# Kernel tuning notes

Hardware: AMD Instinct MI355X
Metric: run time of the kernel (lower is better)

## Reference

```python
import jax, jax.numpy as jnp
from jax import lax
import numpy as np

N, D, K, T, E, S = 2048, 128, 16, 16, 8192, 256
GAMMA, SIGMA, TEMP, EPS = 0.1, 1.0, 1.0, 1e-10


def _xavier(k, out_d, in_d):
    lim = (6.0 / (in_d + out_d)) ** 0.5
    return jax.random.uniform(k, (out_d, in_d), minval=-lim, maxval=lim, dtype=jnp.float32)


def setup_inputs() -> dict:
    key = jax.random.key(0)
    ks = jax.random.split(key, 24)
    inp = {
        'edges': jax.random.randint(ks[0], (T, E, 2), 0, N, dtype=jnp.int32),
        'subject_idx': 3,
        'eps_phi': jax.random.normal(ks[1], (T, N, D), dtype=jnp.float32),
        'eps_beta': jax.random.normal(ks[2], (T, K, D), dtype=jnp.float32),
        'u_gumbel': jax.random.uniform(ks[3], (T, 2 * E, K), dtype=jnp.float32),
        'alpha_mean_emb': jax.random.normal(ks[4], (S, D), dtype=jnp.float32),
        'alpha_std_emb': jax.random.normal(ks[5], (S, D), dtype=jnp.float32),
        'W_s2phi': _xavier(ks[6], N * D, D), 'b_s2phi': jnp.zeros((N * D,), jnp.float32),
        'W_s2beta': _xavier(ks[7], K * D, D), 'b_s2beta': jnp.zeros((K * D,), jnp.float32),
        'W_bmean': _xavier(ks[8], D, D), 'b_bmean': jnp.zeros((D,), jnp.float32),
        'W_bstd': _xavier(ks[9], D, D), 'b_bstd': jnp.zeros((D,), jnp.float32),
        'W_pmean': _xavier(ks[10], D, D), 'b_pmean': jnp.zeros((D,), jnp.float32),
        'W_pstd': _xavier(ks[11], D, D), 'b_pstd': jnp.zeros((D,), jnp.float32),
        'W_pi': _xavier(ks[12], K, D),
        'Wih_n': 0.1 * jax.random.normal(ks[13], (3 * D, 2 * D), dtype=jnp.float32),
        'Whh_n': 0.1 * jax.random.normal(ks[14], (3 * D, D), dtype=jnp.float32),
        'bih_n': jnp.zeros((3 * D,), jnp.float32), 'bhh_n': jnp.zeros((3 * D,), jnp.float32),
        'Wih_c': 0.1 * jax.random.normal(ks[15], (3 * D, 2 * D), dtype=jnp.float32),
        'Whh_c': 0.1 * jax.random.normal(ks[16], (3 * D, D), dtype=jnp.float32),
        'bih_c': jnp.zeros((3 * D,), jnp.float32), 'bhh_c': jnp.zeros((3 * D,), jnp.float32),
        'W_dec': _xavier(ks[17], N, D),
    }
    return inp


def _gru(x, h, Wih, Whh, bih, bhh):
    # torch nn.GRU single-step cell (gate order r, z, n)
    gi = x @ Wih.T + bih
    gh = h @ Whh.T + bhh
    i_r, i_z, i_n = jnp.split(gi, 3, axis=-1)
    h_r, h_z, h_n = jnp.split(gh, 3, axis=-1)
    r = jax.nn.sigmoid(i_r + h_r)
    z = jax.nn.sigmoid(i_z + h_z)
    n = jnp.tanh(i_n + r * h_n)
    return (1.0 - z) * n + z * h


def _kld_gauss(m1, s1, m2, s2):
    # KL(N(m1,s1) || N(m2,s2)), s2 scalar
    return 0.5 * jnp.sum(2.0 * (jnp.log(s2) - jnp.log(s1)) + (s1 ** 2 + (m1 - m2) ** 2) / (s2 ** 2) - 1.0)


def reference(edges, subject_idx, eps_phi, eps_beta, u_gumbel,
              alpha_mean_emb, alpha_std_emb, W_s2phi, b_s2phi, W_s2beta, b_s2beta,
              W_bmean, b_bmean, W_bstd, b_bstd, W_pmean, b_pmean, W_pstd, b_pstd,
              W_pi, Wih_n, Whh_n, bih_n, bhh_n, Wih_c, Whh_c, bih_c, bhh_c, W_dec):
    a_m = alpha_mean_emb[subject_idx]
    a_s = jax.nn.softplus(alpha_std_emb[subject_idx])
    kld_alpha = _kld_gauss(a_m, a_s, jnp.zeros_like(a_m), 1.0)
    phi0 = (a_m @ W_s2phi.T + b_s2phi).reshape(N, D)
    beta0 = (a_m @ W_s2beta.T + b_s2beta).reshape(K, D)

    def step(carry, xs):
        h_phi, h_beta, phi_prior, beta_prior = carry
        e_t, ep, eb, u = xs
        w = jnp.concatenate([e_t[:, 0], e_t[:, 1]])  # [2E]
        c = jnp.concatenate([e_t[:, 1], e_t[:, 0]])  # [2E]
        h_phi = _gru(jnp.concatenate([phi_prior, phi_prior], -1), h_phi, Wih_n, Whh_n, bih_n, bhh_n)
        h_beta = _gru(jnp.concatenate([beta_prior, beta_prior], -1), h_beta, Wih_c, Whh_c, bih_c, bhh_c)
        beta_mean = h_beta @ W_bmean.T + b_bmean
        beta_std = jax.nn.softplus(h_beta @ W_bstd.T + b_bstd)
        phi_mean = h_phi @ W_pmean.T + b_pmean
        phi_std = jax.nn.softplus(h_phi @ W_pstd.T + b_pstd)
        beta_s = beta_mean + beta_std * eb  # [K, D]
        phi_s = phi_mean + phi_std * ep     # [N, D]
        logits_q = (phi_s[w] * phi_s[c]) @ W_pi.T        # [2E, K] posterior logits
        log_post = jax.nn.log_softmax(logits_q, axis=-1)
        post = jnp.exp(log_post)
        log_prior = jax.nn.log_softmax(phi_s[w] @ beta_s.T, axis=-1)  # p(z|w)
        g = -jnp.log(-jnp.log(u + EPS) + EPS)  # gumbel noise
        z = jax.nn.softmax((logits_q + g) / TEMP, axis=-1)  # soft gumbel-softmax sample
        recon_logp = jax.nn.log_softmax((z @ beta_s) @ W_dec.T, axis=-1)  # [2E, N]
        nll = -jnp.sum(jnp.take_along_axis(recon_logp, c[:, None], axis=1))
        kld_z = jnp.sum(post * (log_post - log_prior))
        kld_beta = _kld_gauss(beta_mean, beta_std, beta_prior, GAMMA)
        kld_phi = _kld_gauss(phi_mean, phi_std, phi_prior, SIGMA)
        return (h_phi, h_beta, phi_s, beta_s), jnp.stack([nll, kld_z, kld_beta, kld_phi])

    carry0 = (jnp.zeros((N, D), jnp.float32), jnp.zeros((K, D), jnp.float32), phi0, beta0)
    _, per_t = lax.scan(step, carry0, (edges, eps_phi, eps_beta, u_gumbel))
    sums = per_t.sum(axis=0)  # [nll, kld_z, kld_beta, kld_phi]
    cnt = jnp.float32(T * 2 * E)
    out = jnp.stack([sums[0], sums[1], T * kld_alpha, sums[2], sums[3]]) / cnt
    return out  # [nll, kld_z, kld_alpha, kld_beta, kld_phi]
```

## Files before the change

kernel.cpp:

```cpp
#include <hip/hip_runtime.h>

#define NN 2048
#define DD 128
#define KK 16
#define TT 16
#define EE 8192
#define TWOE 16384
#define CNT 262144.0f

#define LOG2E 1.4426950408889634f
#define LN2   0.6931471805599453f

__device__ __forceinline__ float exp2_(float x) { return __builtin_amdgcn_exp2f(x); }
__device__ __forceinline__ float log2_(float x) { return __builtin_amdgcn_logf(x); }
__device__ __forceinline__ float expf_(float x) { return exp2_(x * LOG2E); }
__device__ __forceinline__ float logf_(float x) { return log2_(x) * LN2; }
__device__ __forceinline__ float sigmoidf_(float x) { return 1.f / (1.f + expf_(-x)); }
__device__ __forceinline__ float softplusf_(float x) { return fmaxf(x, 0.f) + logf_(1.f + expf_(-fabsf(x))); }
__device__ __forceinline__ float tanhf_(float x) { return 1.f - 2.f / (1.f + expf_(2.f * x)); }

#define D4(a,b) ((a).x*(b).x + (a).y*(b).y + (a).z*(b).z + (a).w*(b).w)

__launch_bounds__(256)
__global__ void prep_kernel(const float* __restrict__ Wih_n, const float* __restrict__ Whh_n,
                            const float* __restrict__ Wih_c, const float* __restrict__ Whh_c,
                            const float* __restrict__ W_pmean, const float* __restrict__ W_pstd,
                            const float* __restrict__ W_bmean, const float* __restrict__ W_bstd,
                            float* __restrict__ Bg_n, float* __restrict__ Bg_c,
                            float* __restrict__ Bms_n, float* __restrict__ Bms_c)
{
    int idx = blockIdx.x * 256 + threadIdx.x;
    if (idx < 98304) {
        int r = idx;
        if (r < 49152) { int j = r >> 7, k2 = r & 127; Bg_n[r] = Wih_n[j*256 + k2] + Wih_n[j*256 + 128 + k2]; }
        else Bg_n[r] = Whh_n[r - 49152];
    } else if (idx < 196608) {
        int r = idx - 98304;
        if (r < 49152) { int j = r >> 7, k2 = r & 127; Bg_c[r] = Wih_c[j*256 + k2] + Wih_c[j*256 + 128 + k2]; }
        else Bg_c[r] = Whh_c[r - 49152];
    } else if (idx < 229376) {
        int r = idx - 196608;
        Bms_n[r] = (r < 16384) ? W_pmean[r] : W_pstd[r - 16384];
    } else {
        int r = idx - 229376;
        Bms_c[r] = (r < 16384) ? W_bmean[r] : W_bstd[r - 16384];
    }
}

__launch_bounds__(128)
__global__ void alpha_kernel(const float* __restrict__ amE, const float* __restrict__ asE,
                             const int* __restrict__ sidx, float* __restrict__ a_m, float* __restrict__ acc)
{
    __shared__ float red[128];
    int d = threadIdx.x;
    int s = sidx[0];
    float am = amE[s*128 + d];
    float as = softplusf_(asE[s*128 + d]);
    a_m[d] = am;
    float e = -logf_(as) + 0.5f*(as*as + am*am) - 0.5f;
    red[d] = e; __syncthreads();
    for (int st = 64; st > 0; st >>= 1) { if (d < st) red[d] += red[d + st]; __syncthreads(); }
    if (d == 0) acc[2] = red[0];
}

__launch_bounds__(256)
__global__ void phi0_kernel(const float* __restrict__ Wp, const float* __restrict__ bp,
                            const float* __restrict__ Wb, const float* __restrict__ bb,
                            const float* __restrict__ a_m, float* __restrict__ phi0, float* __restrict__ beta0)
{
    int wid = threadIdx.x >> 6, l = threadIdx.x & 63;
    long long row = (long long)blockIdx.x * 4 + wid;
    const float* W; const float* b; float* o; long long r = row;
    if (row < 262144) { W = Wp; b = bp; o = phi0; }
    else { W = Wb; b = bb; o = beta0; r = row - 262144; }
    const float* wr = W + r * 128;
    float acc = a_m[l] * wr[l] + a_m[64 + l] * wr[64 + l];
    #pragma unroll
    for (int m = 32; m >= 1; m >>= 1) acc += __shfl_xor(acc, m);
    if (l == 0) o[r] = acc + b[r];
}

__launch_bounds__(256)
__global__ void gemm_bias(const float* __restrict__ Ap1, const float* __restrict__ Ap2,
                          const float* __restrict__ Ab1, const float* __restrict__ Ab2,
                          const float* __restrict__ Bphi, const float* __restrict__ Bbeta,
                          const float* __restrict__ b0p, const float* __restrict__ b1p,
                          const float* __restrict__ b0b, const float* __restrict__ b1b,
                          float* __restrict__ Cphi, float* __restrict__ Cbeta,
                          int Ncols, int Nsplit, int MtPhi, int Mbeta)
{
    __shared__ float As[32][68];
    __shared__ float Bs[32][68];
    bool isBeta = (blockIdx.y == (unsigned)MtPhi);
    int n0 = blockIdx.x * 64;
    const float* A = isBeta ? ((n0 >= Nsplit) ? Ab2 : Ab1) : ((n0 >= Nsplit) ? Ap2 : Ap1);
    const float* B = isBeta ? Bbeta : Bphi;
    const float* b0 = isBeta ? b0b : b0p;
    const float* b1 = isBeta ? b1b : b1p;
    float* C = isBeta ? Cbeta : Cphi;
    int M = isBeta ? Mbeta : MtPhi * 64;
    int m0 = isBeta ? 0 : blockIdx.y * 64;
    int tid = threadIdx.x;
    int tx = tid & 15, ty = tid >> 4;
    float accu[4][4] = {};
    int lr = tid >> 2;
    int lk = (tid & 3) * 8;
    for (int k0 = 0; k0 < 128; k0 += 32) {
        int arow = m0 + lr;
        const float* ap = A + (size_t)arow * 128 + k0 + lk;
        const float* bp = B + (size_t)(n0 + lr) * 128 + k0 + lk;
        #pragma unroll
        for (int qq = 0; qq < 8; ++qq) {
            As[lk + qq][lr] = (arow < M) ? ap[qq] : 0.f;
            Bs[lk + qq][lr] = bp[qq];
        }
        __syncthreads();
        #pragma unroll
        for (int kk = 0; kk < 32; ++kk) {
            float av[4], bv[4];
            #pragma unroll
            for (int i2 = 0; i2 < 4; ++i2) av[i2] = As[kk][ty*4 + i2];
            #pragma unroll
            for (int j2 = 0; j2 < 4; ++j2) bv[j2] = Bs[kk][tx*4 + j2];
            #pragma unroll
            for (int i2 = 0; i2 < 4; ++i2)
                #pragma unroll
                for (int j2 = 0; j2 < 4; ++j2)
                    accu[i2][j2] = fmaf(av[i2], bv[j2], accu[i2][j2]);
        }
        __syncthreads();
    }
    #pragma unroll
    for (int i2 = 0; i2 < 4; ++i2) {
        int row = m0 + ty*4 + i2;
        if (row >= M) continue;
        #pragma unroll
        for (int j2 = 0; j2 < 4; ++j2) {
            int col = n0 + tx*4 + j2;
            float bv = (col < Nsplit) ? b0[col] : b1[col - Nsplit];
            C[(size_t)row * Ncols + col] = accu[i2][j2] + bv;
        }
    }
}

__launch_bounds__(256)
__global__ void gates_kernel(const float* __restrict__ Gphi, const float* __restrict__ Gbeta,
                             float* __restrict__ h_phi, float* __restrict__ h_beta)
{
    long long idx = (long long)blockIdx.x * 256 + threadIdx.x;
    const float* G; float* h; int i, jj;
    if (idx < 262144) { i = (int)(idx >> 7); jj = (int)(idx & 127); G = Gphi; h = h_phi; }
    else { int r = (int)(idx - 262144); i = r >> 7; jj = r & 127; G = Gbeta; h = h_beta; }
    const float* g = G + (size_t)i * 768;
    float r_ = sigmoidf_(g[jj] + g[384 + jj]);
    float z_ = sigmoidf_(g[128 + jj] + g[512 + jj]);
    float n_ = tanhf_(g[256 + jj] + r_ * g[640 + jj]);
    int hi = i * 128 + jj;
    h[hi] = (1.f - z_) * n_ + z_ * h[hi];
}

__launch_bounds__(256)
__global__ void sample_kernel(const float* __restrict__ MSphi, const float* __restrict__ MSbeta,
                              const float* __restrict__ epsP, const float* __restrict__ epsB,
                              const float* __restrict__ phiPrior, const float* __restrict__ betaPrior,
                              float* __restrict__ phiS, float* __restrict__ betaS, float* __restrict__ acc)
{
    __shared__ float red[256];
    int tid = threadIdx.x;
    long long idx = (long long)blockIdx.x * 256 + tid;
    float elem; int target;
    if (idx < 262144) {
        int i = (int)(idx >> 7), jj = (int)(idx & 127);
        float mean = MSphi[(size_t)i*256 + jj];
        float stdv = softplusf_(MSphi[(size_t)i*256 + 128 + jj]);
        float sv = mean + stdv * epsP[idx];
        phiS[idx] = sv;
        float d = mean - phiPrior[idx];
        elem = -logf_(stdv) + 0.5f*(stdv*stdv + d*d) - 0.5f;
        target = 4;
    } else {
        int r = (int)(idx - 262144);
        int i = r >> 7, jj = r & 127;
        float mean = MSbeta[i*256 + jj];
        float stdv = softplusf_(MSbeta[i*256 + 128 + jj]);
        float sv = mean + stdv * epsB[r];
        betaS[r] = sv;
        float d = mean - betaPrior[r];
        elem = (-2.3025850929940457f - logf_(stdv)) + 50.0f*(stdv*stdv + d*d) - 0.5f;
        target = 3;
    }
    red[tid] = elem; __syncthreads();
    for (int st = 128; st > 0; st >>= 1) { if (tid < st) red[tid] += red[tid + st]; __syncthreads(); }
    if (tid == 0) atomicAdd(acc + target, red[0]);
}

__launch_bounds__(256)
__global__ void mt_kernel(const float* __restrict__ betaS, const float* __restrict__ W_dec, float* __restrict__ Mt)
{
    int tid = threadIdx.x, wid = tid >> 6, l = tid & 63;
    int n = blockIdx.x * 4 + wid;
    int k = l & 15, q = l >> 4;
    const float* bs = betaS + k*128 + q*32;
    const float* wd = W_dec + (size_t)n*128 + q*32;
    float p = 0.f;
    #pragma unroll
    for (int j = 0; j < 32; ++j) p = fmaf(bs[j], wd[j], p);
    p += __shfl_xor(p, 16);
    p += __shfl_xor(p, 32);
    if (l < 16) Mt[n*16 + l] = p * LOG2E;
}

#define ZSTEP(A,B,Wv,Bv) { float4 a_=(A), b_=(B); \
    lp += a_.x*(Bv).x + a_.y*(Bv).y + a_.z*(Bv).z + a_.w*(Bv).w; \
    lq += (a_.x*b_.x)*(Wv).x + (a_.y*b_.y)*(Wv).y + (a_.z*b_.z)*(Wv).z + (a_.w*b_.w)*(Wv).w; }

__launch_bounds__(256, 3)
__global__ void z_kernel(const float* __restrict__ phiS, const float* __restrict__ betaS,
                         const float* __restrict__ W_pi, const int* __restrict__ edges_t,
                         const float* __restrict__ u_t, float* __restrict__ Z, float* __restrict__ acc)
{
    int tid = threadIdx.x, wid = tid >> 6, l = tid & 63;
    int k = l >> 2, q = l & 3;
    int d0 = q * 32;
    const float4* wp = (const float4*)(W_pi  + k*128 + d0);
    const float4* bp = (const float4*)(betaS + k*128 + d0);
    float4 wr0 = wp[0], wr1 = wp[1], wr2 = wp[2], wr3 = wp[3],
           wr4 = wp[4], wr5 = wp[5], wr6 = wp[6], wr7 = wp[7];
    float4 br0 = bp[0], br1 = bp[1], br2 = bp[2], br3 = bp[3],
           br4 = bp[4], br5 = bp[5], br6 = bp[6], br7 = bp[7];
    float kz = 0.f;
    int gw = blockIdx.x * 4 + wid;
    for (int it = 0; it < 8; ++it) {
        int j = gw * 8 + it;
        int e = j & 8191; int fl = j >> 13;
        int w = edges_t[e*2 + fl], c = edges_t[e*2 + (fl ^ 1)];
        const float4* pw4 = (const float4*)(phiS + w*128 + d0);
        const float4* pc4 = (const float4*)(phiS + c*128 + d0);
        float lq = 0.f, lp = 0.f;
        ZSTEP(pw4[0], pc4[0], wr0, br0); ZSTEP(pw4[1], pc4[1], wr1, br1);
        ZSTEP(pw4[2], pc4[2], wr2, br2); ZSTEP(pw4[3], pc4[3], wr3, br3);
        ZSTEP(pw4[4], pc4[4], wr4, br4); ZSTEP(pw4[5], pc4[5], wr5, br5);
        ZSTEP(pw4[6], pc4[6], wr6, br6); ZSTEP(pw4[7], pc4[7], wr7, br7);
        lq += __shfl_xor(lq, 1); lq += __shfl_xor(lq, 2);
        lp += __shfl_xor(lp, 1); lp += __shfl_xor(lp, 2);
        float eq = expf_(lq);
        float sq = eq;
        sq += __shfl_xor(sq, 4); sq += __shfl_xor(sq, 8); sq += __shfl_xor(sq, 16); sq += __shfl_xor(sq, 32);
        float rsq = __builtin_amdgcn_rcpf(sq);
        float logpost = lq - logf_(sq);
        float post = eq * rsq;
        float mp = lp;
        mp = fmaxf(mp, __shfl_xor(mp, 4));  mp = fmaxf(mp, __shfl_xor(mp, 8));
        mp = fmaxf(mp, __shfl_xor(mp, 16)); mp = fmaxf(mp, __shfl_xor(mp, 32));
        float ep = expf_(lp - mp);
        float sp = ep;
        sp += __shfl_xor(sp, 4); sp += __shfl_xor(sp, 8); sp += __shfl_xor(sp, 16); sp += __shfl_xor(sp, 32);
        float logprior = (lp - mp) - logf_(sp);
        float v = post * (logpost - logprior);
        v += __shfl_xor(v, 4); v += __shfl_xor(v, 8); v += __shfl_xor(v, 16); v += __shfl_xor(v, 32);
        kz += v;
        float u = u_t[(size_t)j*16 + k];
        float g = -logf_(-logf_(u + 1e-10f) + 1e-10f);
        float zl = lq + g;
        float ez = expf_(zl);
        float sz = ez;
        sz += __shfl_xor(sz, 4); sz += __shfl_xor(sz, 8); sz += __shfl_xor(sz, 16); sz += __shfl_xor(sz, 32);
        if (q == 0) Z[(size_t)j*16 + k] = ez * __builtin_amdgcn_rcpf(sz);
    }
    if (l == 0) atomicAdd(acc + 1, kz);
}

__launch_bounds__(512, 3)
__global__ void nll_kernel(const float* __restrict__ Mt, const float* __restrict__ Z,
                           const int* __restrict__ edges_t, float* __restrict__ acc)
{
    __shared__ float ss[32][8], sc[32][8];
    int tid = threadIdx.x, wid = tid >> 6, l = tid & 63;
    int n0 = tid * 4;
    const float4* mp = (const float4*)(Mt + (size_t)n0 * 16);
    float4 M0 = mp[0],  M1 = mp[1],  M2 = mp[2],  M3 = mp[3];
    float4 M4 = mp[4],  M5 = mp[5],  M6 = mp[6],  M7 = mp[7];
    float4 M8 = mp[8],  M9 = mp[9],  M10 = mp[10], M11 = mp[11];
    float4 M12 = mp[12], M13 = mp[13], M14 = mp[14], M15 = mp[15];
    for (int e = 0; e < 32; ++e) {
        int j = blockIdx.x * 32 + e;
        int ei = j & 8191; int fl = j >> 13;
        int c = edges_t[ei*2 + (fl ^ 1)];
        const float4* zp = (const float4*)(Z + (size_t)j * 16);
        float4 Z0 = zp[0], Z1 = zp[1], Z2 = zp[2], Z3 = zp[3];
        float v0 = D4(Z0, M0)  + D4(Z1, M1)  + D4(Z2, M2)  + D4(Z3, M3);
        float v1 = D4(Z0, M4)  + D4(Z1, M5)  + D4(Z2, M6)  + D4(Z3, M7);
        float v2 = D4(Z0, M8)  + D4(Z1, M9)  + D4(Z2, M10) + D4(Z3, M11);
        float v3 = D4(Z0, M12) + D4(Z1, M13) + D4(Z2, M14) + D4(Z3, M15);
        float s = exp2_(v0) + exp2_(v1) + exp2_(v2) + exp2_(v3);
        float cv = 0.f;
        cv = (c == n0    ) ? v0 : cv;
        cv = (c == n0 + 1) ? v1 : cv;
        cv = (c == n0 + 2) ? v2 : cv;
        cv = (c == n0 + 3) ? v3 : cv;
        #pragma unroll
        for (int m = 1; m < 64; m <<= 1) {
            s  += __shfl_xor(s, m);
            cv += __shfl_xor(cv, m);
        }
        if (l == 0) { ss[e][wid] = s; sc[e][wid] = cv; }
    }
    __syncthreads();
    float val = 0.f;
    if (tid < 32) {
        float S = 0.f, CV = 0.f;
        #pragma unroll
        for (int w2 = 0; w2 < 8; ++w2) { S += ss[tid][w2]; CV += sc[tid][w2]; }
        val = LN2 * (log2_(S) - CV);
    }
    if (tid < 64) {
        #pragma unroll
        for (int m = 1; m < 64; m <<= 1) val += __shfl_xor(val, m);
        if (tid == 0) atomicAdd(acc + 0, val);
    }
}

__global__ void final_kernel(const float* __restrict__ acc, float* __restrict__ out)
{
    if (threadIdx.x == 0 && blockIdx.x == 0) {
        out[0] = acc[0] / CNT;
        out[1] = acc[1] / CNT;
        out[2] = 16.f * acc[2] / CNT;
        out[3] = acc[3] / CNT;
        out[4] = acc[4] / CNT;
    }
}

extern "C" void kernel_launch(void* const* d_in, const int* in_sizes, int n_in,
                              void* d_out, int out_size, void* d_ws, size_t ws_size,
                              hipStream_t stream)
{
    (void)in_sizes; (void)n_in; (void)out_size; (void)ws_size;
    const int*   edges   = (const int*)d_in[0];
    const int*   sidx    = (const int*)d_in[1];
    const float* eps_phi = (const float*)d_in[2];
    const float* eps_beta= (const float*)d_in[3];
    const float* u_g     = (const float*)d_in[4];
    const float* amE     = (const float*)d_in[5];
    const float* asE     = (const float*)d_in[6];
    const float* W_s2phi = (const float*)d_in[7];
    const float* b_s2phi = (const float*)d_in[8];
    const float* W_s2beta= (const float*)d_in[9];
    const float* b_s2beta= (const float*)d_in[10];
    const float* W_bmean = (const float*)d_in[11];
    const float* b_bmean = (const float*)d_in[12];
    const float* W_bstd  = (const float*)d_in[13];
    const float* b_bstd  = (const float*)d_in[14];
    const float* W_pmean = (const float*)d_in[15];
    const float* b_pmean = (const float*)d_in[16];
    const float* W_pstd  = (const float*)d_in[17];
    const float* b_pstd  = (const float*)d_in[18];
    const float* W_pi    = (const float*)d_in[19];
    const float* Wih_n   = (const float*)d_in[20];
    const float* Whh_n   = (const float*)d_in[21];
    const float* bih_n   = (const float*)d_in[22];
    const float* bhh_n   = (const float*)d_in[23];
    const float* Wih_c   = (const float*)d_in[24];
    const float* Whh_c   = (const float*)d_in[25];
    const float* bih_c   = (const float*)d_in[26];
    const float* bhh_c   = (const float*)d_in[27];
    const float* W_dec   = (const float*)d_in[28];

    float* ws     = (float*)d_ws;
    float* Bg_n   = ws;
    float* Bg_c   = Bg_n   + 98304;
    float* Bms_n  = Bg_c   + 98304;
    float* Bms_c  = Bms_n  + 32768;
    float* a_m    = Bms_c  + 32768;
    float* phiA   = a_m    + 128;
    float* phiB   = phiA   + 262144;
    float* h_phi  = phiB   + 262144;
    float* betaA  = h_phi  + 262144;
    float* betaB  = betaA  + 2048;
    float* h_beta = betaB  + 2048;
    float* Gphi   = h_beta + 2048;
    float* Gbeta  = Gphi   + 1572864;
    float* MSphi  = Gbeta  + 12288;
    float* MSbeta = MSphi  + 524288;
    float* Mt     = MSbeta + 4096;
    float* Zb     = Mt     + 32768;
    float* acc    = Zb     + 262144;

    (void)hipMemsetAsync(h_phi,  0, 262144 * sizeof(float), stream);
    (void)hipMemsetAsync(h_beta, 0, 2048 * sizeof(float), stream);
    (void)hipMemsetAsync(acc,    0, 8 * sizeof(float), stream);

    prep_kernel<<<1024, 256, 0, stream>>>(Wih_n, Whh_n, Wih_c, Whh_c,
                                          W_pmean, W_pstd, W_bmean, W_bstd,
                                          Bg_n, Bg_c, Bms_n, Bms_c);
    alpha_kernel<<<1, 128, 0, stream>>>(amE, asE, sidx, a_m, acc);
    phi0_kernel<<<66048, 256, 0, stream>>>(W_s2phi, b_s2phi, W_s2beta, b_s2beta, a_m, phiA, betaA);

    float* phiPrior = phiA;  float* phiS = phiB;
    float* betaPrior = betaA; float* betaS = betaB;
    for (int t = 0; t < TT; ++t) {
        gemm_bias<<<dim3(12, 33), 256, 0, stream>>>(phiPrior, h_phi, betaPrior, h_beta,
                                                    Bg_n, Bg_c, bih_n, bhh_n, bih_c, bhh_c,
                                                    Gphi, Gbeta, 768, 384, 32, 16);
        gates_kernel<<<1032, 256, 0, stream>>>(Gphi, Gbeta, h_phi, h_beta);
        gemm_bias<<<dim3(4, 33), 256, 0, stream>>>(h_phi, h_phi, h_beta, h_beta,
                                                   Bms_n, Bms_c, b_pmean, b_pstd, b_bmean, b_bstd,
                                                   MSphi, MSbeta, 256, 128, 32, 16);
        sample_kernel<<<1032, 256, 0, stream>>>(MSphi, MSbeta,
                                                eps_phi + (size_t)t * 262144, eps_beta + (size_t)t * 2048,
                                                phiPrior, betaPrior, phiS, betaS, acc);
        mt_kernel<<<512, 256, 0, stream>>>(betaS, W_dec, Mt);
        z_kernel<<<512, 256, 0, stream>>>(phiS, betaS, W_pi,
                                          edges + (size_t)t * EE * 2, u_g + (size_t)t * TWOE * KK, Zb, acc);
        nll_kernel<<<512, 512, 0, stream>>>(Mt, Zb, edges + (size_t)t * EE * 2, acc);
        float* tp = phiPrior; phiPrior = phiS; phiS = tp;
        float* tb = betaPrior; betaPrior = betaS; betaS = tb;
    }
    final_kernel<<<1, 64, 0, stream>>>(acc, (float*)d_out);
}
```

Measured before the change: 2.682 ms.

## Fuse GRU gemm with gates, mean/std gemm with sampling, and z with nll

The per-step pipeline drops from seven kernels to four. The GRU input and hidden GEMMs are now fused with the gate nonlinearity, with ping-pong hidden buffers. The mean/std GEMM is fused with reparameterised sampling and the KL reduction. The z and nll kernels are merged so soft samples stay in shared memory, and the alpha, prep and memset setup work is folded into one init kernel. This removes the large G, MS and Z global intermediates and several launches per step. The trade-off is that the fused GEMMs launch only 132 blocks each, which lowers parallelism.

```diff
diff --git a/kernel.cpp b/kernel.cpp
--- a/kernel.cpp
+++ b/kernel.cpp
@@ -22,14 +22,36 @@
 #define D4(a,b) ((a).x*(b).x + (a).y*(b).y + (a).z*(b).z + (a).w*(b).w)
 
 __launch_bounds__(256)
-__global__ void prep_kernel(const float* __restrict__ Wih_n, const float* __restrict__ Whh_n,
+__global__ void init_kernel(const float* __restrict__ Wih_n, const float* __restrict__ Whh_n,
                             const float* __restrict__ Wih_c, const float* __restrict__ Whh_c,
                             const float* __restrict__ W_pmean, const float* __restrict__ W_pstd,
                             const float* __restrict__ W_bmean, const float* __restrict__ W_bstd,
                             float* __restrict__ Bg_n, float* __restrict__ Bg_c,
-                            float* __restrict__ Bms_n, float* __restrict__ Bms_c)
-{
+                            float* __restrict__ Bms_n, float* __restrict__ Bms_c,
+                            float* __restrict__ hphiA, float* __restrict__ hbetaA,
+                            const float* __restrict__ amE, const float* __restrict__ asE,
+                            const int* __restrict__ sidx, float* __restrict__ a_m,
+                            float* __restrict__ acc)
+{
+    if (blockIdx.x == 1024) {
+        __shared__ float red[128];
+        int d = threadIdx.x;
+        if (d < 128) {
+            int s = sidx[0];
+            float am = amE[s*128 + d];
+            float as = softplusf_(asE[s*128 + d]);
+            a_m[d] = am;
+            red[d] = -logf_(as) + 0.5f*(as*as + am*am) - 0.5f;
+        }
+        __syncthreads();
+        for (int st = 64; st > 0; st >>= 1) { if (d < st) red[d] += red[d + st]; __syncthreads(); }
+        if (d == 0) acc[2] = red[0];
+        return;
+    }
     int idx = blockIdx.x * 256 + threadIdx.x;
+    hphiA[idx] = 0.f;
+    if (idx < 2048) hbetaA[idx] = 0.f;
+    if (idx < 2) { acc[idx] = 0.f; acc[idx + 3] = 0.f; }
     if (idx < 98304) {
         int r = idx;
         if (r < 49152) { int j = r >> 7, k2 = r & 127; Bg_n[r] = Wih_n[j*256 + k2] + Wih_n[j*256 + 128 + k2]; }
@@ -47,22 +69,6 @@
     }
 }
 
-__launch_bounds__(128)
-__global__ void alpha_kernel(const float* __restrict__ amE, const float* __restrict__ asE,
-                             const int* __restrict__ sidx, float* __restrict__ a_m, float* __restrict__ acc)
-{
-    __shared__ float red[128];
-    int d = threadIdx.x;
-    int s = sidx[0];
-    float am = amE[s*128 + d];
-    float as = softplusf_(asE[s*128 + d]);
-    a_m[d] = am;
-    float e = -logf_(as) + 0.5f*(as*as + am*am) - 0.5f;
-    red[d] = e; __syncthreads();
-    for (int st = 64; st > 0; st >>= 1) { if (d < st) red[d] += red[d + st]; __syncthreads(); }
-    if (d == 0) acc[2] = red[0];
-}
-
 __launch_bounds__(256)
 __global__ void phi0_kernel(const float* __restrict__ Wp, const float* __restrict__ bp,
                             const float* __restrict__ Wb, const float* __restrict__ bb,
@@ -81,117 +87,172 @@
 }
 
 __launch_bounds__(256)
-__global__ void gemm_bias(const float* __restrict__ Ap1, const float* __restrict__ Ap2,
-                          const float* __restrict__ Ab1, const float* __restrict__ Ab2,
-                          const float* __restrict__ Bphi, const float* __restrict__ Bbeta,
-                          const float* __restrict__ b0p, const float* __restrict__ b1p,
-                          const float* __restrict__ b0b, const float* __restrict__ b1b,
-                          float* __restrict__ Cphi, float* __restrict__ Cbeta,
-                          int Ncols, int Nsplit, int MtPhi, int Mbeta)
-{
-    __shared__ float As[32][68];
-    __shared__ float Bs[32][68];
-    bool isBeta = (blockIdx.y == (unsigned)MtPhi);
-    int n0 = blockIdx.x * 64;
-    const float* A = isBeta ? ((n0 >= Nsplit) ? Ab2 : Ab1) : ((n0 >= Nsplit) ? Ap2 : Ap1);
-    const float* B = isBeta ? Bbeta : Bphi;
-    const float* b0 = isBeta ? b0b : b0p;
-    const float* b1 = isBeta ? b1b : b1p;
-    float* C = isBeta ? Cbeta : Cphi;
-    int M = isBeta ? Mbeta : MtPhi * 64;
-    int m0 = isBeta ? 0 : blockIdx.y * 64;
+__global__ void gru_kernel(const float* __restrict__ phiPrior, const float* __restrict__ betaPrior,
+                           const float* __restrict__ hPhiOld, float* __restrict__ hPhiNew,
+                           const float* __restrict__ hBetaOld, float* __restrict__ hBetaNew,
+                           const float* __restrict__ Bg_n, const float* __restrict__ Bg_c,
+                           const float* __restrict__ bih_n, const float* __restrict__ bhh_n,
+                           const float* __restrict__ bih_c, const float* __restrict__ bhh_c)
+{
+    __shared__ float Xs[32][64];
+    __shared__ float Hs[32][64];
+    __shared__ float Ws[32][192];
+    int bx = blockIdx.x;
+    const float* X; const float* Hold; float* Hnew; const float* Bg; const float* bih; const float* bhh;
+    int m0, M, j0;
+    if (bx < 128) {
+        m0 = (bx >> 2) * 64; j0 = (bx & 3) * 32; M = 2048;
+        X = phiPrior; Hold = hPhiOld; Hnew = hPhiNew; Bg = Bg_n; bih = bih_n; bhh = bhh_n;
+    } else {
+        m0 = 0; j0 = (bx - 128) * 32; M = 16;
+        X = betaPrior; Hold = hBetaOld; Hnew = hBetaNew; Bg = Bg_c; bih = bih_c; bhh = bhh_c;
+    }
     int tid = threadIdx.x;
-    int tx = tid & 15, ty = tid >> 4;
-    float accu[4][4] = {};
-    int lr = tid >> 2;
-    int lk = (tid & 3) * 8;
+    int j  = tid & 31;
+    int rr = tid >> 5;
+    float acc[6][8] = {};
+    int srow = tid >> 3;
+    int skq  = (tid & 7) * 4;
     for (int k0 = 0; k0 < 128; k0 += 32) {
-        int arow = m0 + lr;
-        const float* ap = A + (size_t)arow * 128 + k0 + lk;
-        const float* bp = B + (size_t)(n0 + lr) * 128 + k0 + lk;
-        #pragma unroll
-        for (int qq = 0; qq < 8; ++qq) {
-            As[lk + qq][lr] = (arow < M) ? ap[qq] : 0.f;
-            Bs[lk + qq][lr] = bp[qq];
+        #pragma unroll
+        for (int h2 = 0; h2 < 2; ++h2) {
+            int row = srow + 32 * h2;
+            int grow = m0 + row;
+            float4 xv = make_float4(0.f,0.f,0.f,0.f), hv = xv;
+            if (grow < M) {
+                xv = *(const float4*)(X    + (size_t)grow*128 + k0 + skq);
+                hv = *(const float4*)(Hold + (size_t)grow*128 + k0 + skq);
+            }
+            Xs[skq+0][row] = xv.x; Xs[skq+1][row] = xv.y; Xs[skq+2][row] = xv.z; Xs[skq+3][row] = xv.w;
+            Hs[skq+0][row] = hv.x; Hs[skq+1][row] = hv.y; Hs[skq+2][row] = hv.z; Hs[skq+3][row] = hv.w;
+        }
+        #pragma unroll
+        for (int h6 = 0; h6 < 6; ++h6) {
+            int rowIdx = srow + 32 * h6;
+            int g = rowIdx >> 5, jj2 = rowIdx & 31;
+            float4 wv = *(const float4*)(Bg + (size_t)(g*128 + j0 + jj2)*128 + k0 + skq);
+            Ws[skq+0][rowIdx] = wv.x; Ws[skq+1][rowIdx] = wv.y; Ws[skq+2][rowIdx] = wv.z; Ws[skq+3][rowIdx] = wv.w;
         }
         __syncthreads();
         #pragma unroll
         for (int kk = 0; kk < 32; ++kk) {
-            float av[4], bv[4];
+            float xa[8], ha[8];
+            *(float4*)&xa[0] = *(const float4*)&Xs[kk][rr*8];
+            *(float4*)&xa[4] = *(const float4*)&Xs[kk][rr*8+4];
+            *(float4*)&ha[0] = *(const float4*)&Hs[kk][rr*8];
+            *(float4*)&ha[4] = *(const float4*)&Hs[kk][rr*8+4];
             #pragma unroll
-            for (int i2 = 0; i2 < 4; ++i2) av[i2] = As[kk][ty*4 + i2];
+            for (int g = 0; g < 3; ++g) {
+                float wv = Ws[kk][g*32 + j];
+                #pragma unroll
+                for (int i = 0; i < 8; ++i) acc[g][i] = fmaf(xa[i], wv, acc[g][i]);
+            }
             #pragma unroll
-            for (int j2 = 0; j2 < 4; ++j2) bv[j2] = Bs[kk][tx*4 + j2];
+            for (int g = 3; g < 6; ++g) {
+                float wv = Ws[kk][g*32 + j];
+                #pragma unroll
+                for (int i = 0; i < 8; ++i) acc[g][i] = fmaf(ha[i], wv, acc[g][i]);
+            }
+        }
+        __syncthreads();
+    }
+    float bi_r = bih[j0 + j], bi_z = bih[128 + j0 + j], bi_n = bih[256 + j0 + j];
+    float bh_r = bhh[j0 + j], bh_z = bhh[128 + j0 + j], bh_n = bhh[256 + j0 + j];
+    #pragma unroll
+    for (int i = 0; i < 8; ++i) {
+        int row = m0 + rr*8 + i;
+        if (row < M) {
+            float r_ = sigmoidf_(acc[0][i] + bi_r + acc[3][i] + bh_r);
+            float z_ = sigmoidf_(acc[1][i] + bi_z + acc[4][i] + bh_z);
+            float n_ = tanhf_(acc[2][i] + bi_n + r_ * (acc[5][i] + bh_n));
+            size_t hi = (size_t)row * 128 + j0 + j;
+            Hnew[hi] = (1.f - z_) * n_ + z_ * Hold[hi];
+        }
+    }
+}
+
+__launch_bounds__(256)
+__global__ void ms_kernel(const float* __restrict__ hPhi, const float* __restrict__ hBeta,
+                          const float* __restrict__ Bms_n, const float* __restrict__ Bms_c,
+                          const float* __restrict__ b_pmean, const float* __restrict__ b_pstd,
+                          const float* __restrict__ b_bmean, const float* __restrict__ b_bstd,
+                          const float* __restrict__ epsP, const float* __restrict__ epsB,
+                          const float* __restrict__ phiPrior, const float* __restrict__ betaPrior,
+                          float* __restrict__ phiS, float* __restrict__ betaS, float* __restrict__ acc)
+{
+    __shared__ float Hs[32][64];
+    __shared__ float Wms[32][64];
+    __shared__ float red[256];
+    int bx = blockIdx.x;
+    const float* H; const float* Bms; const float* bm; const float* bs;
+    const float* eps; const float* prior; float* out;
+    int m0, M, j0; bool isPhi;
+    if (bx < 128) {
+        m0 = (bx >> 2) * 64; j0 = (bx & 3) * 32; M = 2048; isPhi = true;
+        H = hPhi; Bms = Bms_n; bm = b_pmean; bs = b_pstd; eps = epsP; prior = phiPrior; out = phiS;
+    } else {
+        m0 = 0; j0 = (bx - 128) * 32; M = 16; isPhi = false;
+        H = hBeta; Bms = Bms_c; bm = b_bmean; bs = b_bstd; eps = epsB; prior = betaPrior; out = betaS;
+    }
+    int tid = threadIdx.x;
+    int j  = tid & 31;
+    int rr = tid >> 5;
+    float accM[8] = {}, accS[8] = {};
+    int srow = tid >> 3;
+    int skq  = (tid & 7) * 4;
+    for (int k0 = 0; k0 < 128; k0 += 32) {
+        #pragma unroll
+        for (int h2 = 0; h2 < 2; ++h2) {
+            int row = srow + 32 * h2;
+            int grow = m0 + row;
+            float4 hv = make_float4(0.f,0.f,0.f,0.f);
+            if (grow < M) hv = *(const float4*)(H + (size_t)grow*128 + k0 + skq);
+            Hs[skq+0][row] = hv.x; Hs[skq+1][row] = hv.y; Hs[skq+2][row] = hv.z; Hs[skq+3][row] = hv.w;
+        }
+        {
+            int rowIdx = srow + 32 * 0;
             #pragma unroll
-            for (int i2 = 0; i2 < 4; ++i2)
-                #pragma unroll
-                for (int j2 = 0; j2 < 4; ++j2)
-                    accu[i2][j2] = fmaf(av[i2], bv[j2], accu[i2][j2]);
+            for (int h2 = 0; h2 < 2; ++h2) {
+                int ri = rowIdx + 32 * h2;
+                int grp = ri >> 5, jj2 = ri & 31;
+                float4 wv = *(const float4*)(Bms + (size_t)(grp*128 + j0 + jj2)*128 + k0 + skq);
+                Wms[skq+0][ri] = wv.x; Wms[skq+1][ri] = wv.y; Wms[skq+2][ri] = wv.z; Wms[skq+3][ri] = wv.w;
+            }
         }
         __syncthreads();
-    }
+        #pragma unroll
+        for (int kk = 0; kk < 32; ++kk) {
+            float hv[8];
+            *(float4*)&hv[0] = *(const float4*)&Hs[kk][rr*8];
+            *(float4*)&hv[4] = *(const float4*)&Hs[kk][rr*8+4];
+            float wm = Wms[kk][j];
+            float ws = Wms[kk][32 + j];
+            #pragma unroll
+            for (int i = 0; i < 8; ++i) {
+                accM[i] = fmaf(hv[i], wm, accM[i]);
+                accS[i] = fmaf(hv[i], ws, accS[i]);
+            }
+        }
+        __syncthreads();
+    }
+    float bmv = bm[j0 + j], bsv = bs[j0 + j];
+    float kld = 0.f;
     #pragma unroll
-    for (int i2 = 0; i2 < 4; ++i2) {
-        int row = m0 + ty*4 + i2;
-        if (row >= M) continue;
-        #pragma unroll
-        for (int j2 = 0; j2 < 4; ++j2) {
-            int col = n0 + tx*4 + j2;
-            float bv = (col < Nsplit) ? b0[col] : b1[col - Nsplit];
-            C[(size_t)row * Ncols + col] = accu[i2][j2] + bv;
-        }
-    }
-}
-
-__launch_bounds__(256)
-__global__ void gates_kernel(const float* __restrict__ Gphi, const float* __restrict__ Gbeta,
-                             float* __restrict__ h_phi, float* __restrict__ h_beta)
-{
-    long long idx = (long long)blockIdx.x * 256 + threadIdx.x;
-    const float* G; float* h; int i, jj;
-    if (idx < 262144) { i = (int)(idx >> 7); jj = (int)(idx & 127); G = Gphi; h = h_phi; }
-    else { int r = (int)(idx - 262144); i = r >> 7; jj = r & 127; G = Gbeta; h = h_beta; }
-    const float* g = G + (size_t)i * 768;
-    float r_ = sigmoidf_(g[jj] + g[384 + jj]);
-    float z_ = sigmoidf_(g[128 + jj] + g[512 + jj]);
-    float n_ = tanhf_(g[256 + jj] + r_ * g[640 + jj]);
-    int hi = i * 128 + jj;
-    h[hi] = (1.f - z_) * n_ + z_ * h[hi];
-}
-
-__launch_bounds__(256)
-__global__ void sample_kernel(const float* __restrict__ MSphi, const float* __restrict__ MSbeta,
-                              const float* __restrict__ epsP, const float* __restrict__ epsB,
-                              const float* __restrict__ phiPrior, const float* __restrict__ betaPrior,
-                              float* __restrict__ phiS, float* __restrict__ betaS, float* __restrict__ acc)
-{
-    __shared__ float red[256];
-    int tid = threadIdx.x;
-    long long idx = (long long)blockIdx.x * 256 + tid;
-    float elem; int target;
-    if (idx < 262144) {
-        int i = (int)(idx >> 7), jj = (int)(idx & 127);
-        float mean = MSphi[(size_t)i*256 + jj];
-        float stdv = softplusf_(MSphi[(size_t)i*256 + 128 + jj]);
-        float sv = mean + stdv * epsP[idx];
-        phiS[idx] = sv;
-        float d = mean - phiPrior[idx];
-        elem = -logf_(stdv) + 0.5f*(stdv*stdv + d*d) - 0.5f;
-        target = 4;
-    } else {
-        int r = (int)(idx - 262144);
-        int i = r >> 7, jj = r & 127;
-        float mean = MSbeta[i*256 + jj];
-        float stdv = softplusf_(MSbeta[i*256 + 128 + jj]);
-        float sv = mean + stdv * epsB[r];
-        betaS[r] = sv;
-        float d = mean - betaPrior[r];
-        elem = (-2.3025850929940457f - logf_(stdv)) + 50.0f*(stdv*stdv + d*d) - 0.5f;
-        target = 3;
-    }
-    red[tid] = elem; __syncthreads();
+    for (int i = 0; i < 8; ++i) {
+        int row = m0 + rr*8 + i;
+        if (row < M) {
+            size_t gi = (size_t)row * 128 + j0 + j;
+            float mean = accM[i] + bmv;
+            float stdv = softplusf_(accS[i] + bsv);
+            out[gi] = mean + stdv * eps[gi];
+            float d = mean - prior[gi];
+            if (isPhi) kld += -logf_(stdv) + 0.5f*(stdv*stdv + d*d) - 0.5f;
+            else       kld += (-2.3025850929940457f - logf_(stdv)) + 50.0f*(stdv*stdv + d*d) - 0.5f;
+        }
+    }
+    red[tid] = kld; __syncthreads();
     for (int st = 128; st > 0; st >>= 1) { if (tid < st) red[tid] += red[tid + st]; __syncthreads(); }
-    if (tid == 0) atomicAdd(acc + target, red[0]);
+    if (tid == 0) atomicAdd(acc + (isPhi ? 4 : 3), red[0]);
 }
 
 __launch_bounds__(256)
@@ -204,7 +265,7 @@
     const float* wd = W_dec + (size_t)n*128 + q*32;
     float p = 0.f;
     #pragma unroll
-    for (int j = 0; j < 32; ++j) p = fmaf(bs[j], wd[j], p);
+    for (int jj = 0; jj < 32; ++jj) p = fmaf(bs[jj], wd[jj], p);
     p += __shfl_xor(p, 16);
     p += __shfl_xor(p, 32);
     if (l < 16) Mt[n*16 + l] = p * LOG2E;
@@ -214,80 +275,85 @@
     lp += a_.x*(Bv).x + a_.y*(Bv).y + a_.z*(Bv).z + a_.w*(Bv).w; \
     lq += (a_.x*b_.x)*(Wv).x + (a_.y*b_.y)*(Wv).y + (a_.z*b_.z)*(Wv).z + (a_.w*b_.w)*(Wv).w; }
 
-__launch_bounds__(256, 3)
-__global__ void z_kernel(const float* __restrict__ phiS, const float* __restrict__ betaS,
-                         const float* __restrict__ W_pi, const int* __restrict__ edges_t,
-                         const float* __restrict__ u_t, float* __restrict__ Z, float* __restrict__ acc)
-{
+__launch_bounds__(512, 2)
+__global__ void znll_kernel(const float* __restrict__ phiS, const float* __restrict__ betaS,
+                            const float* __restrict__ W_pi, const float* __restrict__ Mt,
+                            const int* __restrict__ edges_t, const float* __restrict__ u_t,
+                            float* __restrict__ acc)
+{
+    __shared__ float zbuf[64][16];
+    __shared__ float ss[64][8], sc[64][8];
+    __shared__ int   cbuf[64];
+    __shared__ float kred[8];
     int tid = threadIdx.x, wid = tid >> 6, l = tid & 63;
-    int k = l >> 2, q = l & 3;
-    int d0 = q * 32;
-    const float4* wp = (const float4*)(W_pi  + k*128 + d0);
-    const float4* bp = (const float4*)(betaS + k*128 + d0);
-    float4 wr0 = wp[0], wr1 = wp[1], wr2 = wp[2], wr3 = wp[3],
-           wr4 = wp[4], wr5 = wp[5], wr6 = wp[6], wr7 = wp[7];
-    float4 br0 = bp[0], br1 = bp[1], br2 = bp[2], br3 = bp[3],
-           br4 = bp[4], br5 = bp[5], br6 = bp[6], br7 = bp[7];
-    float kz = 0.f;
-    int gw = blockIdx.x * 4 + wid;
-    for (int it = 0; it < 8; ++it) {
-        int j = gw * 8 + it;
-        int e = j & 8191; int fl = j >> 13;
-        int w = edges_t[e*2 + fl], c = edges_t[e*2 + (fl ^ 1)];
-        const float4* pw4 = (const float4*)(phiS + w*128 + d0);
-        const float4* pc4 = (const float4*)(phiS + c*128 + d0);
-        float lq = 0.f, lp = 0.f;
-        ZSTEP(pw4[0], pc4[0], wr0, br0); ZSTEP(pw4[1], pc4[1], wr1, br1);
-        ZSTEP(pw4[2], pc4[2], wr2, br2); ZSTEP(pw4[3], pc4[3], wr3, br3);
-        ZSTEP(pw4[4], pc4[4], wr4, br4); ZSTEP(pw4[5], pc4[5], wr5, br5);
-        ZSTEP(pw4[6], pc4[6], wr6, br6); ZSTEP(pw4[7], pc4[7], wr7, br7);
-        lq += __shfl_xor(lq, 1); lq += __shfl_xor(lq, 2);
-        lp += __shfl_xor(lp, 1); lp += __shfl_xor(lp, 2);
-        float eq = expf_(lq);
-        float sq = eq;
-        sq += __shfl_xor(sq, 4); sq += __shfl_xor(sq, 8); sq += __shfl_xor(sq, 16); sq += __shfl_xor(sq, 32);
-        float rsq = __builtin_amdgcn_rcpf(sq);
-        float logpost = lq - logf_(sq);
-        float post = eq * rsq;
-        float mp = lp;
-        mp = fmaxf(mp, __shfl_xor(mp, 4));  mp = fmaxf(mp, __shfl_xor(mp, 8));
-        mp = fmaxf(mp, __shfl_xor(mp, 16)); mp = fmaxf(mp, __shfl_xor(mp, 32));
-        float ep = expf_(lp - mp);
-        float sp = ep;
-        sp += __shfl_xor(sp, 4); sp += __shfl_xor(sp, 8); sp += __shfl_xor(sp, 16); sp += __shfl_xor(sp, 32);
-        float logprior = (lp - mp) - logf_(sp);
-        float v = post * (logpost - logprior);
-        v += __shfl_xor(v, 4); v += __shfl_xor(v, 8); v += __shfl_xor(v, 16); v += __shfl_xor(v, 32);
-        kz += v;
-        float u = u_t[(size_t)j*16 + k];
-        float g = -logf_(-logf_(u + 1e-10f) + 1e-10f);
-        float zl = lq + g;
-        float ez = expf_(zl);
-        float sz = ez;
-        sz += __shfl_xor(sz, 4); sz += __shfl_xor(sz, 8); sz += __shfl_xor(sz, 16); sz += __shfl_xor(sz, 32);
-        if (q == 0) Z[(size_t)j*16 + k] = ez * __builtin_amdgcn_rcpf(sz);
-    }
-    if (l == 0) atomicAdd(acc + 1, kz);
-}
-
-__launch_bounds__(512, 3)
-__global__ void nll_kernel(const float* __restrict__ Mt, const float* __restrict__ Z,
-                           const int* __restrict__ edges_t, float* __restrict__ acc)
-{
-    __shared__ float ss[32][8], sc[32][8];
-    int tid = threadIdx.x, wid = tid >> 6, l = tid & 63;
+    {
+        int k = l >> 2, q = l & 3;
+        int d0 = q * 32;
+        const float4* wp = (const float4*)(W_pi  + k*128 + d0);
+        const float4* bp = (const float4*)(betaS + k*128 + d0);
+        float4 wr0 = wp[0], wr1 = wp[1], wr2 = wp[2], wr3 = wp[3],
+               wr4 = wp[4], wr5 = wp[5], wr6 = wp[6], wr7 = wp[7];
+        float4 br0 = bp[0], br1 = bp[1], br2 = bp[2], br3 = bp[3],
+               br4 = bp[4], br5 = bp[5], br6 = bp[6], br7 = bp[7];
+        float kz = 0.f;
+        #pragma unroll
+        for (int it = 0; it < 8; ++it) {
+            int jl = wid * 8 + it;
+            int j = blockIdx.x * 64 + jl;
+            int e = j & 8191; int fl = j >> 13;
+            int w = edges_t[e*2 + fl], c = edges_t[e*2 + (fl ^ 1)];
+            const float4* pw4 = (const float4*)(phiS + (size_t)w*128 + d0);
+            const float4* pc4 = (const float4*)(phiS + (size_t)c*128 + d0);
+            float lq = 0.f, lp = 0.f;
+            ZSTEP(pw4[0], pc4[0], wr0, br0); ZSTEP(pw4[1], pc4[1], wr1, br1);
+            ZSTEP(pw4[2], pc4[2], wr2, br2); ZSTEP(pw4[3], pc4[3], wr3, br3);
+            ZSTEP(pw4[4], pc4[4], wr4, br4); ZSTEP(pw4[5], pc4[5], wr5, br5);
+            ZSTEP(pw4[6], pc4[6], wr6, br6); ZSTEP(pw4[7], pc4[7], wr7, br7);
+            lq += __shfl_xor(lq, 1); lq += __shfl_xor(lq, 2);
+            lp += __shfl_xor(lp, 1); lp += __shfl_xor(lp, 2);
+            float eq = expf_(lq);
+            float sq = eq;
+            sq += __shfl_xor(sq, 4); sq += __shfl_xor(sq, 8); sq += __shfl_xor(sq, 16); sq += __shfl_xor(sq, 32);
+            float logpost = lq - logf_(sq);
+            float post = eq * __builtin_amdgcn_rcpf(sq);
+            float mp = lp;
+            mp = fmaxf(mp, __shfl_xor(mp, 4));  mp = fmaxf(mp, __shfl_xor(mp, 8));
+            mp = fmaxf(mp, __shfl_xor(mp, 16)); mp = fmaxf(mp, __shfl_xor(mp, 32));
+            float ep = expf_(lp - mp);
+            float sp = ep;
+            sp += __shfl_xor(sp, 4); sp += __shfl_xor(sp, 8); sp += __shfl_xor(sp, 16); sp += __shfl_xor(sp, 32);
+            float logprior = (lp - mp) - logf_(sp);
+            float v = post * (logpost - logprior);
+            v += __shfl_xor(v, 4); v += __shfl_xor(v, 8); v += __shfl_xor(v, 16); v += __shfl_xor(v, 32);
+            kz += v;
+            float u = u_t[(size_t)j*16 + k];
+            float g = -logf_(-logf_(u + 1e-10f) + 1e-10f);
+            float zl = lq + g;
+            float ez = expf_(zl);
+            float sz = ez;
+            sz += __shfl_xor(sz, 4); sz += __shfl_xor(sz, 8); sz += __shfl_xor(sz, 16); sz += __shfl_xor(sz, 32);
+            if (q == 0) zbuf[jl][k] = ez * __builtin_amdgcn_rcpf(sz);
+            if (l == 0) cbuf[jl] = c;
+        }
+        if (l == 0) kred[wid] = kz;
+    }
+    __syncthreads();
+    if (tid == 0) {
+        float t = 0.f;
+        #pragma unroll
+        for (int w2 = 0; w2 < 8; ++w2) t += kred[w2];
+        atomicAdd(acc + 1, t);
+    }
     int n0 = tid * 4;
-    const float4* mp = (const float4*)(Mt + (size_t)n0 * 16);
-    float4 M0 = mp[0],  M1 = mp[1],  M2 = mp[2],  M3 = mp[3];
-    float4 M4 = mp[4],  M5 = mp[5],  M6 = mp[6],  M7 = mp[7];
-    float4 M8 = mp[8],  M9 = mp[9],  M10 = mp[10], M11 = mp[11];
-    float4 M12 = mp[12], M13 = mp[13], M14 = mp[14], M15 = mp[15];
-    for (int e = 0; e < 32; ++e) {
-        int j = blockIdx.x * 32 + e;
-        int ei = j & 8191; int fl = j >> 13;
-        int c = edges_t[ei*2 + (fl ^ 1)];
-        const float4* zp = (const float4*)(Z + (size_t)j * 16);
+    const float4* mp4 = (const float4*)(Mt + (size_t)n0 * 16);
+    float4 M0 = mp4[0],  M1 = mp4[1],  M2 = mp4[2],  M3 = mp4[3];
+    float4 M4 = mp4[4],  M5 = mp4[5],  M6 = mp4[6],  M7 = mp4[7];
+    float4 M8 = mp4[8],  M9 = mp4[9],  M10 = mp4[10], M11 = mp4[11];
+    float4 M12 = mp4[12], M13 = mp4[13], M14 = mp4[14], M15 = mp4[15];
+    for (int e = 0; e < 64; ++e) {
+        const float4* zp = (const float4*)&zbuf[e][0];
         float4 Z0 = zp[0], Z1 = zp[1], Z2 = zp[2], Z3 = zp[3];
+        int c = cbuf[e];
         float v0 = D4(Z0, M0)  + D4(Z1, M1)  + D4(Z2, M2)  + D4(Z3, M3);
         float v1 = D4(Z0, M4)  + D4(Z1, M5)  + D4(Z2, M6)  + D4(Z3, M7);
         float v2 = D4(Z0, M8)  + D4(Z1, M9)  + D4(Z2, M10) + D4(Z3, M11);
@@ -306,14 +372,11 @@
         if (l == 0) { ss[e][wid] = s; sc[e][wid] = cv; }
     }
     __syncthreads();
-    float val = 0.f;
-    if (tid < 32) {
+    if (tid < 64) {
         float S = 0.f, CV = 0.f;
         #pragma unroll
         for (int w2 = 0; w2 < 8; ++w2) { S += ss[tid][w2]; CV += sc[tid][w2]; }
-        val = LN2 * (log2_(S) - CV);
-    }
-    if (tid < 64) {
+        float val = LN2 * (log2_(S) - CV);
         #pragma unroll
         for (int m = 1; m < 64; m <<= 1) val += __shfl_xor(val, m);
         if (tid == 0) atomicAdd(acc + 0, val);
@@ -374,47 +437,40 @@
     float* a_m    = Bms_c  + 32768;
     float* phiA   = a_m    + 128;
     float* phiB   = phiA   + 262144;
-    float* h_phi  = phiB   + 262144;
-    float* betaA  = h_phi  + 262144;
+    float* hphiA  = phiB   + 262144;
+    float* hphiB  = hphiA  + 262144;
+    float* betaA  = hphiB  + 262144;
     float* betaB  = betaA  + 2048;
-    float* h_beta = betaB  + 2048;
-    float* Gphi   = h_beta + 2048;
-    float* Gbeta  = Gphi   + 1572864;
-    float* MSphi  = Gbeta  + 12288;
-    float* MSbeta = MSphi  + 524288;
-    float* Mt     = MSbeta + 4096;
-    float* Zb     = Mt     + 32768;
-    float* acc    = Zb     + 262144;
-
-    (void)hipMemsetAsync(h_phi,  0, 262144 * sizeof(float), stream);
-    (void)hipMemsetAsync(h_beta, 0, 2048 * sizeof(float), stream);
-    (void)hipMemsetAsync(acc,    0, 8 * sizeof(float), stream);
-
-    prep_kernel<<<1024, 256, 0, stream>>>(Wih_n, Whh_n, Wih_c, Whh_c,
+    float* hbetaA = betaB  + 2048;
+    float* hbetaB = hbetaA + 2048;
+    float* Mt     = hbetaB + 2048;
+    float* acc    = Mt     + 32768;
+
+    init_kernel<<<1025, 256, 0, stream>>>(Wih_n, Whh_n, Wih_c, Whh_c,
                                           W_pmean, W_pstd, W_bmean, W_bstd,
-                                          Bg_n, Bg_c, Bms_n, Bms_c);
-    alpha_kernel<<<1, 128, 0, stream>>>(amE, asE, sidx, a_m, acc);
+                                          Bg_n, Bg_c, Bms_n, Bms_c,
+                                          hphiA, hbetaA, amE, asE, sidx, a_m, acc);
     phi0_kernel<<<66048, 256, 0, stream>>>(W_s2phi, b_s2phi, W_s2beta, b_s2beta, a_m, phiA, betaA);
 
     float* phiPrior = phiA;  float* phiS = phiB;
     float* betaPrior = betaA; float* betaS = betaB;
+    float* hPhiOld = hphiA;  float* hPhiNew = hphiB;
+    float* hBetaOld = hbetaA; float* hBetaNew = hbetaB;
     for (int t = 0; t < TT; ++t) {
-        gemm_bias<<<dim3(12, 33), 256, 0, stream>>>(phiPrior, h_phi, betaPrior, h_beta,
-                                                    Bg_n, Bg_c, bih_n, bhh_n, bih_c, bhh_c,
-                                                    Gphi, Gbeta, 768, 384, 32, 16);
-        gates_kernel<<<1032, 256, 0, stream>>>(Gphi, Gbeta, h_phi, h_beta);
-        gemm_bias<<<dim3(4, 33), 256, 0, stream>>>(h_phi, h_phi, h_beta, h_beta,
-                                                   Bms_n, Bms_c, b_pmean, b_pstd, b_bmean, b_bstd,
-                                                   MSphi, MSbeta, 256, 128, 32, 16);
-        sample_kernel<<<1032, 256, 0, stream>>>(MSphi, MSbeta,
-                                                eps_phi + (size_t)t * 262144, eps_beta + (size_t)t * 2048,
-                                                phiPrior, betaPrior, phiS, betaS, acc);
+        gru_kernel<<<132, 256, 0, stream>>>(phiPrior, betaPrior,
+                                            hPhiOld, hPhiNew, hBetaOld, hBetaNew,
+                                            Bg_n, Bg_c, bih_n, bhh_n, bih_c, bhh_c);
+        ms_kernel<<<132, 256, 0, stream>>>(hPhiNew, hBetaNew, Bms_n, Bms_c,
+                                           b_pmean, b_pstd, b_bmean, b_bstd,
+                                           eps_phi + (size_t)t * 262144, eps_beta + (size_t)t * 2048,
+                                           phiPrior, betaPrior, phiS, betaS, acc);
         mt_kernel<<<512, 256, 0, stream>>>(betaS, W_dec, Mt);
-        z_kernel<<<512, 256, 0, stream>>>(phiS, betaS, W_pi,
-                                          edges + (size_t)t * EE * 2, u_g + (size_t)t * TWOE * KK, Zb, acc);
-        nll_kernel<<<512, 512, 0, stream>>>(Mt, Zb, edges + (size_t)t * EE * 2, acc);
+        znll_kernel<<<256, 512, 0, stream>>>(phiS, betaS, W_pi, Mt,
+                                             edges + (size_t)t * EE * 2, u_g + (size_t)t * TWOE * KK, acc);
         float* tp = phiPrior; phiPrior = phiS; phiS = tp;
         float* tb = betaPrior; betaPrior = betaS; betaS = tb;
+        float* th = hPhiOld; hPhiOld = hPhiNew; hPhiNew = th;
+        float* tb2 = hBetaOld; hBetaOld = hBetaNew; hBetaNew = tb2;
     }
     final_kernel<<<1, 64, 0, stream>>>(acc, (float*)d_out);
 }
```

Result: faster. 2.194 ms (-18.2%).
